# Optimization experiments

Measured on AMD Instinct MI355X. Metric: run time of the kernel, lower is better.

Reference implementation:

```python
import jax, jax.numpy as jnp
import numpy as np

N1, N2, F = 512, 512, 128
H = 512  # hidden width


def _xavier(key, shape):
    fan_in, fan_out = shape
    std = (2.0 / (fan_in + fan_out)) ** 0.5
    return jax.random.normal(key, shape, dtype=jnp.float32) * std


def setup_inputs() -> dict:
    key = jax.random.key(0)
    ks = jax.random.split(key, 8)
    V1 = jax.random.normal(ks[0], (1, N1, F), dtype=jnp.float32)
    V2 = jax.random.normal(ks[1], (1, N2, F), dtype=jnp.float32)
    W1 = _xavier(ks[2], (2 * F, H))
    b1 = 0.0001 + 5e-05 * jax.random.normal(ks[3], (H,), dtype=jnp.float32)
    W2 = _xavier(ks[4], (H, H))
    b2 = 0.0001 + 5e-05 * jax.random.normal(ks[5], (H,), dtype=jnp.float32)
    W3 = _xavier(ks[6], (H, 2))
    b3 = 0.0001 + 5e-05 * jax.random.normal(ks[7], (2,), dtype=jnp.float32)
    return {"V1": V1, "V2": V2, "W1": W1, "b1": b1, "W2": W2, "b2": b2, "W3": W3, "b3": b3}


def reference(V1, V2, W1, b1, W2, b2, W3, b3):
    n1, n2, f = V1.shape[1], V2.shape[1], V1.shape[2]
    # Fused broadcast-concat replacing the N1*N2 Python double loop
    # (i outer, j inner; V1[i] first, V2[j] second -> row-major reshape matches stack order)
    pairs = jnp.concatenate([
        jnp.broadcast_to(V1[0][:, None, :], (n1, n2, f)),
        jnp.broadcast_to(V2[0][None, :, :], (n1, n2, f)),
    ], axis=-1).reshape(1, n1 * n2, 2 * f)
    h = jax.nn.relu(pairs @ W1 + b1)
    h = jax.nn.relu(h @ W2 + b2)
    out = jax.nn.relu(h @ W3 + b3)  # final LinearEmbedding also has ReLU by default
    return out
```

## Files before the change

### kernel.cpp

```cpp
#include <hip/hip_runtime.h>


typedef short bf16x8 __attribute__((ext_vector_type(8)));
typedef float f32x4 __attribute__((ext_vector_type(4)));

#define NROW 512
#define FDIM 128
#define HDIM 512

__device__ __forceinline__ unsigned short f2bf(float x) {
  unsigned int u = __builtin_bit_cast(unsigned int, x);
  u += 0x7fffu + ((u >> 16) & 1u);
  return (unsigned short)(u >> 16);
}
__device__ __forceinline__ unsigned int pk2(float x, float y) {
  return (unsigned)f2bf(x) | ((unsigned)f2bf(y) << 16);
}

__global__ __launch_bounds__(256) void prep_ab(
    const float* __restrict__ V1, const float* __restrict__ V2,
    const float* __restrict__ W1, const float* __restrict__ b1,
    float* __restrict__ Ap, float* __restrict__ Bp) {
  __shared__ float sv[4 * FDIM];
  const int b = blockIdx.x;
  const int t = threadIdx.x;
  const bool isB = b >= 128;
  const int r0 = (b & 127) * 4;
  const float* V = isB ? V2 : V1;
  const float* W = W1 + (isB ? FDIM * HDIM : 0);
  for (int idx = t; idx < 4 * FDIM; idx += 256) sv[idx] = V[r0 * FDIM + idx];
  __syncthreads();
  float s[4][2] = {};
  for (int k = 0; k < FDIM; ++k) {
    const float w0 = W[k * HDIM + t];
    const float w1 = W[k * HDIM + t + 256];
#pragma unroll
    for (int r = 0; r < 4; ++r) {
      const float v = sv[r * FDIM + k];
      s[r][0] += v * w0;
      s[r][1] += v * w1;
    }
  }
  float* O = isB ? Bp : Ap;
  const float bb0 = isB ? 0.f : b1[t];
  const float bb1 = isB ? 0.f : b1[t + 256];
#pragma unroll
  for (int r = 0; r < 4; ++r) {
    O[(r0 + r) * HDIM + t] = s[r][0] + bb0;
    O[(r0 + r) * HDIM + t + 256] = s[r][1] + bb1;
  }
}

__global__ __launch_bounds__(256) void prep_w2(const float* __restrict__ W2,
                                               unsigned short* __restrict__ W2T) {
  const int o = blockIdx.x * 256 + threadIdx.x;
  const int kt = o >> 12;
  const int s = (o >> 9) & 7;
  const int n = o & 511;
  const int kb = kt * 64 + s * 8;
  unsigned int u[4];
#pragma unroll
  for (int e2 = 0; e2 < 4; ++e2) {
    const unsigned short lo = f2bf(W2[(kb + 2 * e2) * HDIM + n]);
    const unsigned short hi = f2bf(W2[(kb + 2 * e2 + 1) * HDIM + n]);
    u[e2] = (unsigned)lo | ((unsigned)hi << 16);
  }
  *(uint4*)(W2T + (size_t)o * 8) = make_uint4(u[0], u[1], u[2], u[3]);
}

__global__ __launch_bounds__(512, 4) void mlp_main(
    const float* __restrict__ Ap, const float* __restrict__ Bp,
    const unsigned short* __restrict__ W2T, const float* __restrict__ b2,
    const float* __restrict__ W3, const float* __restrict__ b3,
    float* __restrict__ out) {
  extern __shared__ char smem[];
  char* sA = smem;
  float* sP = (float*)(smem + 65536);

  const int tid = threadIdx.x;
  const int wave = tid >> 6;
  const int lane = tid & 63;
  const int lane15 = lane & 15;
  const int kgrp = lane >> 4;
  const int sw = lane15 & 7;

  const int m0 = blockIdx.x * 64;
  const int i = m0 >> 9;
  const int j0 = m0 & 511;

  {
    const int c = tid & 63;
    const int rsub = tid >> 6;
    const float4 a0 = *(const float4*)(Ap + i * HDIM + c * 8);
    const float4 a1 = *(const float4*)(Ap + i * HDIM + c * 8 + 4);
#pragma unroll
    for (int it = 0; it < 8; ++it) {
      const int row = it * 8 + rsub;
      const float4 g0 = *(const float4*)(Bp + (size_t)(j0 + row) * HDIM + c * 8);
      const float4 g1 = *(const float4*)(Bp + (size_t)(j0 + row) * HDIM + c * 8 + 4);
      const uint4 v = make_uint4(
          pk2(fmaxf(a0.x + g0.x, 0.f), fmaxf(a0.y + g0.y, 0.f)),
          pk2(fmaxf(a0.z + g0.z, 0.f), fmaxf(a0.w + g0.w, 0.f)),
          pk2(fmaxf(a1.x + g1.x, 0.f), fmaxf(a1.y + g1.y, 0.f)),
          pk2(fmaxf(a1.z + g1.z, 0.f), fmaxf(a1.w + g1.w, 0.f)));
      *(uint4*)(sA + row * 1024 + ((c ^ (row & 7)) << 4)) = v;
    }
  }
  __syncthreads();

  f32x4 acc[4][4];
#pragma unroll
  for (int mt = 0; mt < 4; ++mt)
#pragma unroll
    for (int nt = 0; nt < 4; ++nt) acc[mt][nt] = (f32x4){0.f, 0.f, 0.f, 0.f};

  const char* bbase = (const char*)W2T + (((kgrp << 9) + (wave << 6) + lane15) << 4);

  bf16x8 bf[2][4];
#pragma unroll
  for (int nt = 0; nt < 4; ++nt) bf[0][nt] = *(const bf16x8*)(bbase + (nt << 8));

#pragma unroll
  for (int s = 0; s < 16; ++s) {
    const int cur = s & 1;
    if (s < 15) {
      const char* p = bbase + ((s + 1) << 15);
#pragma unroll
      for (int nt = 0; nt < 4; ++nt) bf[cur ^ 1][nt] = *(const bf16x8*)(p + (nt << 8));
    }
    const int kt = s >> 1;
    const int ks = s & 1;
    const int csel = ((ks << 2) | kgrp) ^ sw;
    bf16x8 af[4];
#pragma unroll
    for (int mt = 0; mt < 4; ++mt) {
      const int row = mt * 16 + lane15;
      af[mt] = *(const bf16x8*)(sA + row * 1024 + (((kt << 3) | csel) << 4));
    }
#pragma unroll
    for (int nt = 0; nt < 4; ++nt)
#pragma unroll
      for (int mt = 0; mt < 4; ++mt)
        acc[mt][nt] =
            __builtin_amdgcn_mfma_f32_16x16x32_bf16(af[mt], bf[cur][nt], acc[mt][nt], 0, 0, 0);
  }

  float w30[4], w31[4], bbv[4];
#pragma unroll
  for (int nt = 0; nt < 4; ++nt) {
    const int n = (wave << 6) + (nt << 4) + lane15;
    w30[nt] = W3[2 * n];
    w31[nt] = W3[2 * n + 1];
    bbv[nt] = b2[n];
  }
#pragma unroll
  for (int mt = 0; mt < 4; ++mt) {
    float p[4][2] = {};
#pragma unroll
    for (int nt = 0; nt < 4; ++nt)
#pragma unroll
      for (int q = 0; q < 4; ++q) {
        const float h = fmaxf(acc[mt][nt][q] + bbv[nt], 0.f);
        p[q][0] += h * w30[nt];
        p[q][1] += h * w31[nt];
      }
#pragma unroll
    for (int d = 1; d < 16; d <<= 1)
#pragma unroll
      for (int q = 0; q < 4; ++q) {
        p[q][0] += __shfl_xor(p[q][0], d, 64);
        p[q][1] += __shfl_xor(p[q][1], d, 64);
      }
    if (lane15 == 0) {
#pragma unroll
      for (int q = 0; q < 4; ++q) {
        const int r = mt * 16 + kgrp * 4 + q;
        sP[(wave * 64 + r) * 2 + 0] = p[q][0];
        sP[(wave * 64 + r) * 2 + 1] = p[q][1];
      }
    }
  }
  __syncthreads();
  if (tid < 128) {
    const int r = tid >> 1;
    const int c = tid & 1;
    float v = b3[c];
#pragma unroll
    for (int w = 0; w < 8; ++w) v += sP[(w * 64 + r) * 2 + c];
    out[((m0 + r) << 1) + c] = fmaxf(v, 0.f);
  }
}

extern "C" void kernel_launch(void* const* d_in, const int* in_sizes, int n_in,
                              void* d_out, int out_size, void* d_ws, size_t ws_size,
                              hipStream_t stream) {
  const float* V1 = (const float*)d_in[0];
  const float* V2 = (const float*)d_in[1];
  const float* W1 = (const float*)d_in[2];
  const float* b1 = (const float*)d_in[3];
  const float* W2 = (const float*)d_in[4];
  const float* b2 = (const float*)d_in[5];
  const float* W3 = (const float*)d_in[6];
  const float* b3 = (const float*)d_in[7];

  float* Ap = (float*)d_ws;
  float* Bp = Ap + NROW * HDIM;
  unsigned short* W2T = (unsigned short*)(Bp + NROW * HDIM);

  const int smem_bytes = 65536 + 8 * 64 * 2 * 4;
  (void)hipFuncSetAttribute((const void*)mlp_main,
                            hipFuncAttributeMaxDynamicSharedMemorySize, smem_bytes);

  prep_ab<<<256, 256, 0, stream>>>(V1, V2, W1, b1, Ap, Bp);
  prep_w2<<<128, 256, 0, stream>>>(W2, W2T);
  mlp_main<<<4096, 512, smem_bytes, stream>>>(Ap, Bp, W2T, b2, W3, b3, (float*)d_out);
}
```

Baseline: 168.8 us.

## Switch to 32x32x16 MFMA with new W2 layout and smem-based epilogue reduction

Replaces the 16x16x32 bf16 MFMA tiling (4x4 tiles per wave) with 32x32x16 MFMA (2x2 tiles per wave). To match, it re-lays out the W2 bf16 pack as simple k-chunks of 8, widens the LDS swizzle to 16, and double-buffers both A fragments from LDS and B fragments from global memory. It also adds s_setprio around the MFMA block and rewrites the epilogue as a cross-wave reduction through the reused A shared buffer, which removes the separate partial-sum buffer. The aim is fewer, larger MFMA instructions and fewer LDS reads per FLOP. The cost is extra barriers in the epilogue and a different register-pressure profile.

```diff
diff --git a/kernel.cpp b/kernel.cpp
--- a/kernel.cpp
+++ b/kernel.cpp
@@ -2,7 +2,7 @@
 
 
 typedef short bf16x8 __attribute__((ext_vector_type(8)));
-typedef float f32x4 __attribute__((ext_vector_type(4)));
+typedef float f32x16 __attribute__((ext_vector_type(16)));
 
 #define NROW 512
 #define FDIM 128
@@ -54,15 +54,13 @@
 __global__ __launch_bounds__(256) void prep_w2(const float* __restrict__ W2,
                                                unsigned short* __restrict__ W2T) {
   const int o = blockIdx.x * 256 + threadIdx.x;
-  const int kt = o >> 12;
-  const int s = (o >> 9) & 7;
+  const int kc = o >> 9;
   const int n = o & 511;
-  const int kb = kt * 64 + s * 8;
   unsigned int u[4];
 #pragma unroll
   for (int e2 = 0; e2 < 4; ++e2) {
-    const unsigned short lo = f2bf(W2[(kb + 2 * e2) * HDIM + n]);
-    const unsigned short hi = f2bf(W2[(kb + 2 * e2 + 1) * HDIM + n]);
+    const unsigned short lo = f2bf(W2[(kc * 8 + 2 * e2) * HDIM + n]);
+    const unsigned short hi = f2bf(W2[(kc * 8 + 2 * e2 + 1) * HDIM + n]);
     u[e2] = (unsigned)lo | ((unsigned)hi << 16);
   }
   *(uint4*)(W2T + (size_t)o * 8) = make_uint4(u[0], u[1], u[2], u[3]);
@@ -75,14 +73,13 @@
     float* __restrict__ out) {
   extern __shared__ char smem[];
   char* sA = smem;
-  float* sP = (float*)(smem + 65536);
 
   const int tid = threadIdx.x;
   const int wave = tid >> 6;
   const int lane = tid & 63;
-  const int lane15 = lane & 15;
-  const int kgrp = lane >> 4;
-  const int sw = lane15 & 7;
+  const int cl = lane & 31;
+  const int hi = lane >> 5;
+  const int r15 = lane & 15;
 
   const int m0 = blockIdx.x * 64;
   const int i = m0 >> 9;
@@ -103,91 +100,97 @@
           pk2(fmaxf(a0.z + g0.z, 0.f), fmaxf(a0.w + g0.w, 0.f)),
           pk2(fmaxf(a1.x + g1.x, 0.f), fmaxf(a1.y + g1.y, 0.f)),
           pk2(fmaxf(a1.z + g1.z, 0.f), fmaxf(a1.w + g1.w, 0.f)));
-      *(uint4*)(sA + row * 1024 + ((c ^ (row & 7)) << 4)) = v;
+      *(uint4*)(sA + row * 1024 + ((c ^ (row & 15)) << 4)) = v;
     }
   }
   __syncthreads();
 
-  f32x4 acc[4][4];
-#pragma unroll
-  for (int mt = 0; mt < 4; ++mt)
-#pragma unroll
-    for (int nt = 0; nt < 4; ++nt) acc[mt][nt] = (f32x4){0.f, 0.f, 0.f, 0.f};
-
-  const char* bbase = (const char*)W2T + (((kgrp << 9) + (wave << 6) + lane15) << 4);
-
-  bf16x8 bf[2][4];
-#pragma unroll
-  for (int nt = 0; nt < 4; ++nt) bf[0][nt] = *(const bf16x8*)(bbase + (nt << 8));
-
-#pragma unroll
-  for (int s = 0; s < 16; ++s) {
+  f32x16 acc[2][2];
+#pragma unroll
+  for (int mt = 0; mt < 2; ++mt)
+#pragma unroll
+    for (int nt = 0; nt < 2; ++nt)
+#pragma unroll
+      for (int q = 0; q < 16; ++q) acc[mt][nt][q] = 0.f;
+
+  const char* abase0 = sA + cl * 1024;
+  const char* bbase = (const char*)W2T + (((wave << 6) + cl) << 4) + (hi << 13);
+
+  bf16x8 af[2][2], bfr[2][2];
+  {
+    const int off = (hi ^ r15) << 4;
+    af[0][0] = *(const bf16x8*)(abase0 + off);
+    af[0][1] = *(const bf16x8*)(abase0 + 32768 + off);
+    bfr[0][0] = *(const bf16x8*)(bbase);
+    bfr[0][1] = *(const bf16x8*)(bbase + (1 << 9));
+  }
+#pragma unroll
+  for (int s = 0; s < 32; ++s) {
     const int cur = s & 1;
-    if (s < 15) {
-      const char* p = bbase + ((s + 1) << 15);
-#pragma unroll
-      for (int nt = 0; nt < 4; ++nt) bf[cur ^ 1][nt] = *(const bf16x8*)(p + (nt << 8));
-    }
-    const int kt = s >> 1;
-    const int ks = s & 1;
-    const int csel = ((ks << 2) | kgrp) ^ sw;
-    bf16x8 af[4];
-#pragma unroll
-    for (int mt = 0; mt < 4; ++mt) {
-      const int row = mt * 16 + lane15;
-      af[mt] = *(const bf16x8*)(sA + row * 1024 + (((kt << 3) | csel) << 4));
-    }
-#pragma unroll
-    for (int nt = 0; nt < 4; ++nt)
-#pragma unroll
-      for (int mt = 0; mt < 4; ++mt)
-        acc[mt][nt] =
-            __builtin_amdgcn_mfma_f32_16x16x32_bf16(af[mt], bf[cur][nt], acc[mt][nt], 0, 0, 0);
-  }
-
-  float w30[4], w31[4], bbv[4];
-#pragma unroll
-  for (int nt = 0; nt < 4; ++nt) {
-    const int n = (wave << 6) + (nt << 4) + lane15;
+    const int nxt = cur ^ 1;
+    if (s < 31) {
+      const int off = ((((s + 1) << 1) | hi) ^ r15) << 4;
+      af[nxt][0] = *(const bf16x8*)(abase0 + off);
+      af[nxt][1] = *(const bf16x8*)(abase0 + 32768 + off);
+      const char* bp = bbase + ((size_t)(s + 1) << 14);
+      bfr[nxt][0] = *(const bf16x8*)(bp);
+      bfr[nxt][1] = *(const bf16x8*)(bp + (1 << 9));
+    }
+    __builtin_amdgcn_s_setprio(1);
+#pragma unroll
+    for (int nt = 0; nt < 2; ++nt)
+#pragma unroll
+      for (int mt = 0; mt < 2; ++mt)
+        acc[mt][nt] = __builtin_amdgcn_mfma_f32_32x32x16_bf16(af[cur][mt], bfr[cur][nt],
+                                                              acc[mt][nt], 0, 0, 0);
+    __builtin_amdgcn_s_setprio(0);
+  }
+
+  __syncthreads();
+
+  float w30[2], w31[2], bb[2];
+#pragma unroll
+  for (int nt = 0; nt < 2; ++nt) {
+    const int n = (wave << 6) + (nt << 5) + cl;
     w30[nt] = W3[2 * n];
     w31[nt] = W3[2 * n + 1];
-    bbv[nt] = b2[n];
-  }
-#pragma unroll
-  for (int mt = 0; mt < 4; ++mt) {
-    float p[4][2] = {};
-#pragma unroll
-    for (int nt = 0; nt < 4; ++nt)
-#pragma unroll
-      for (int q = 0; q < 4; ++q) {
-        const float h = fmaxf(acc[mt][nt][q] + bbv[nt], 0.f);
-        p[q][0] += h * w30[nt];
-        p[q][1] += h * w31[nt];
+    bb[nt] = b2[n];
+  }
+  const float bb3_0 = b3[0], bb3_1 = b3[1];
+
+  for (int mt = 0; mt < 2; ++mt) {
+#pragma unroll
+    for (int reg = 0; reg < 16; ++reg) {
+      const float h0 = fmaxf(acc[mt][0][reg] + bb[0], 0.f);
+      const float h1 = fmaxf(acc[mt][1][reg] + bb[1], 0.f);
+      const float p0 = h0 * w30[0] + h1 * w30[1];
+      const float p1 = h0 * w31[0] + h1 * w31[1];
+      const int r = (reg & 3) + ((reg >> 2) << 3) + (hi << 2);
+      *(float2*)(smem + r * 2048 + (((wave << 5) + cl) << 3)) = make_float2(p0, p1);
+    }
+    __syncthreads();
+    {
+      const int r = tid >> 4;
+      const int sub = tid & 15;
+      float s0 = 0.f, s1 = 0.f;
+#pragma unroll
+      for (int k = 0; k < 16; ++k) {
+        const int kk = (k + sub) & 15;
+        const float2 v = *(const float2*)(smem + r * 2048 + (((sub << 4) + kk) << 3));
+        s0 += v.x;
+        s1 += v.y;
       }
 #pragma unroll
-    for (int d = 1; d < 16; d <<= 1)
-#pragma unroll
-      for (int q = 0; q < 4; ++q) {
-        p[q][0] += __shfl_xor(p[q][0], d, 64);
-        p[q][1] += __shfl_xor(p[q][1], d, 64);
+      for (int d = 1; d < 16; d <<= 1) {
+        s0 += __shfl_xor(s0, d, 64);
+        s1 += __shfl_xor(s1, d, 64);
       }
-    if (lane15 == 0) {
-#pragma unroll
-      for (int q = 0; q < 4; ++q) {
-        const int r = mt * 16 + kgrp * 4 + q;
-        sP[(wave * 64 + r) * 2 + 0] = p[q][0];
-        sP[(wave * 64 + r) * 2 + 1] = p[q][1];
+      if (sub == 0) {
+        const int rg = m0 + (mt << 5) + r;
+        *(float2*)(out + rg * 2) = make_float2(fmaxf(s0 + bb3_0, 0.f), fmaxf(s1 + bb3_1, 0.f));
       }
     }
-  }
-  __syncthreads();
-  if (tid < 128) {
-    const int r = tid >> 1;
-    const int c = tid & 1;
-    float v = b3[c];
-#pragma unroll
-    for (int w = 0; w < 8; ++w) v += sP[(w * 64 + r) * 2 + c];
-    out[((m0 + r) << 1) + c] = fmaxf(v, 0.f);
+    __syncthreads();
   }
 }
 
@@ -207,7 +210,7 @@
   float* Bp = Ap + NROW * HDIM;
   unsigned short* W2T = (unsigned short*)(Bp + NROW * HDIM);
 
-  const int smem_bytes = 65536 + 8 * 64 * 2 * 4;
+  const int smem_bytes = 65536;
   (void)hipFuncSetAttribute((const void*)mlp_main,
                             hipFuncAttributeMaxDynamicSharedMemorySize, smem_bytes);
 
```

Measured after the change: 163.1 us. 1.03x faster.
